# Kernel tuning notes

Hardware: AMD Instinct MI355X
Metric: run time of the kernel (lower is better)

## Reference

```python
import jax, jax.numpy as jnp
import numpy as np

B, N, D = 8, 2048, 1024
DC = 1024          # d_center
K = 4              # num_centers
NUM_JUMPS = 2
SPAN = 2
FIN = (2 + 2 * NUM_JUMPS + 1) * D  # 7*D

def _gelu(x):
    return jax.nn.gelu(x, approximate=False)  # torch nn.GELU default is exact erf

def setup_inputs() -> dict:
    key = jax.random.key(0)
    ks = jax.random.split(key, 16)
    s = lambda k, *sh: jax.random.normal(k, sh, dtype=jnp.float32) * 0.02
    return {
        "queries": jax.random.normal(ks[0], (B, N, D), dtype=jnp.float32),
        "fr_w1": s(ks[1], FIN, D), "fr_b1": jnp.zeros((D,), jnp.float32),
        "fr_w2": s(ks[2], D, D),   "fr_b2": jnp.zeros((D,), jnp.float32),
        "tc_w1": s(ks[3], D, DC),  "tc_b1": jnp.zeros((DC,), jnp.float32),
        "tc_w2": s(ks[4], DC, DC), "tc_b2": jnp.zeros((DC,), jnp.float32),
        "centers": jax.random.normal(ks[5], (K, DC), dtype=jnp.float32),
        "fc_w1": s(ks[6], D + DC, D), "fc_b1": jnp.zeros((D,), jnp.float32),
        "fc_w2": s(ks[7], D, D),      "fc_b2": jnp.zeros((D,), jnp.float32),
        "g_w": s(ks[8], D + DC, D),   "g_b": jnp.zeros((D,), jnp.float32),
    }

def reference(queries, fr_w1, fr_b1, fr_w2, fr_b2,
              tc_w1, tc_b1, tc_w2, tc_b2, centers,
              fc_w1, fc_b1, fc_w2, fc_b2, g_w, g_b):
    x = queries
    shifts = [1, -1, 0]  # left, right, x
    for i in range(1, NUM_JUMPS + 1):
        shifts += [i * SPAN, -i * SPAN]
    fusion = jnp.concatenate([jnp.roll(x, s, axis=1) for s in shifts], axis=-1)  # [B,N,7D]
    x_ring = _gelu(fusion @ fr_w1 + fr_b1) @ fr_w2 + fr_b2                       # [B,N,D]
    token_proj = _gelu(x_ring @ tc_w1 + tc_b1) @ tc_w2 + tc_b2                   # [B,N,DC]
    w = jax.nn.softmax(jnp.einsum('bnd,kd->bnk', token_proj, centers), axis=-1)  # [B,N,K]
    weighted = jnp.einsum('bnk,kd->bnd', w, centers)                             # [B,N,DC]
    fus2 = jnp.concatenate([x_ring, weighted], axis=-1)                          # [B,N,D+DC]
    gate = jax.nn.sigmoid(fus2 @ g_w + g_b)
    fc = _gelu(fus2 @ fc_w1 + fc_b1) @ fc_w2 + fc_b2
    return gate * fc + (1.0 - gate) * x_ring
```

## Files before the change

kernel.cpp:

```cpp
#include <hip/hip_runtime.h>
#include <hip/hip_bf16.h>
#include <math.h>

typedef unsigned short u16;
typedef __attribute__((ext_vector_type(8))) short short8;
typedef __attribute__((ext_vector_type(4))) float f32x4;


__device__ __forceinline__ float bf2f(u16 b) {
  return __uint_as_float(((unsigned int)b) << 16);
}
__device__ __forceinline__ u16 f2bf(float f) {
  unsigned int u = __float_as_uint(f);
  u += 0x7FFFu + ((u >> 16) & 1u);
  return (u16)(u >> 16);
}
__device__ __forceinline__ float gelu_exact(float x) {
  return 0.5f * x * (1.0f + erff(x * 0.70710678118654752f));
}

__device__ __forceinline__ void cp16(const void* g, void* l) {
  __builtin_amdgcn_global_load_lds(
      (const __attribute__((address_space(1))) unsigned int*)g,
      (__attribute__((address_space(3))) unsigned int*)l, 16, 0, 0);
}

template <int MODE, bool GATHER>
__global__ __launch_bounds__(256) void gemm128(
    const u16* __restrict__ A, int lda, const u16* __restrict__ Wt, int K,
    const float* __restrict__ bias, const float* __restrict__ bias2,
    void* __restrict__ out0, int ldo0, void* __restrict__ out1,
    void* __restrict__ out2, const float* __restrict__ p0,
    const float* __restrict__ p1, const float* __restrict__ p2) {
  __shared__ __align__(16) u16 As[128 * 64];
  __shared__ __align__(16) u16 Bs[128 * 64];

  const int tid = threadIdx.x;
  const int lane = tid & 63;
  const int wave = tid >> 6;
  const int wm = wave >> 1;
  const int wn = wave & 1;

  const unsigned linear = blockIdx.y * gridDim.x + blockIdx.x;
  const unsigned xcd = linear & 7u;
  const unsigned pos = linear >> 3;
  const unsigned bx = pos % gridDim.x;
  const unsigned by = xcd * (gridDim.y >> 3) + pos / gridDim.x;
  const int m0 = by * 128;
  const int n0 = bx * 128;

  const int srow = lane >> 3;
  const int sq = lane & 7;
  const int sqs = sq ^ srow;

  f32x4 acc[4][4];
#pragma unroll
  for (int i = 0; i < 4; i++)
#pragma unroll
    for (int j = 0; j < 4; j++) acc[i][j] = (f32x4){0.f, 0.f, 0.f, 0.f};

  for (int k0 = 0; k0 < K; k0 += 64) {
#pragma unroll
    for (int i = 0; i < 4; i++) {
      const int rloc = wave * 32 + i * 8 + srow;
      long gofs;
      if (GATHER) {
        const int seg = k0 >> 10;
        int shift;
        switch (seg) {
          case 0: shift = 1; break;
          case 1: shift = -1; break;
          case 2: shift = 0; break;
          case 3: shift = 2; break;
          case 4: shift = -2; break;
          case 5: shift = 4; break;
          default: shift = -4; break;
        }
        const int m = m0 + rloc;
        const int b = m >> 11;
        const int nsrc = ((m & 2047) - shift) & 2047;
        gofs = (long)((b << 11) | nsrc) * 1024 + (k0 & 1023) + sqs * 8;
      } else {
        gofs = (long)(m0 + rloc) * lda + k0 + sqs * 8;
      }
      cp16(A + gofs, &As[(wave * 32 + i * 8) * 64]);
    }
#pragma unroll
    for (int i = 0; i < 4; i++) {
      const int rloc = wave * 32 + i * 8 + srow;
      const long gofs = (long)(n0 + rloc) * K + k0 + sqs * 8;
      cp16(Wt + gofs, &Bs[(wave * 32 + i * 8) * 64]);
    }
    __syncthreads();

    const int q4 = lane >> 4;
    const int r16 = lane & 15;
#pragma unroll
    for (int kk = 0; kk < 2; kk++) {
      short8 af[4], bf[4];
#pragma unroll
      for (int mi = 0; mi < 4; mi++) {
        const int row = wm * 64 + mi * 16 + r16;
        const int q = (kk * 4 + q4) ^ (row & 7);
        af[mi] = *(const short8*)&As[row * 64 + q * 8];
      }
#pragma unroll
      for (int ni = 0; ni < 4; ni++) {
        const int row = wn * 64 + ni * 16 + r16;
        const int q = (kk * 4 + q4) ^ (row & 7);
        bf[ni] = *(const short8*)&Bs[row * 64 + q * 8];
      }
#pragma unroll
      for (int mi = 0; mi < 4; mi++)
#pragma unroll
        for (int ni = 0; ni < 4; ni++)
          acc[mi][ni] = __builtin_amdgcn_mfma_f32_16x16x32_bf16(
              af[mi], bf[ni], acc[mi][ni], 0, 0, 0);
    }
    __syncthreads();
  }

  const int ccol = lane & 15;
  const int crow = (lane >> 4) * 4;
#pragma unroll
  for (int mi = 0; mi < 4; mi++) {
#pragma unroll
    for (int r = 0; r < 4; r++) {
      const int m = m0 + wm * 64 + mi * 16 + crow + r;
      float4 wrow;
      if (MODE == 8) wrow = *(const float4*)(p0 + (size_t)m * 4);
#pragma unroll
      for (int ni = 0; ni < 4; ni++) {
        const int n = n0 + wn * 64 + ni * 16 + ccol;
        const float v = acc[mi][ni][r];
        if (MODE == 0) {
          ((u16*)out0)[(long)m * ldo0 + n] = f2bf(gelu_exact(v + bias[n]));
        } else if (MODE == 4) {
          const float g = p0[(long)m * 1024 + n];
          const float xr = p1[(long)m * 1024 + n];
          ((float*)out0)[(long)m * ldo0 + n] =
              g * (v + bias[n]) + (1.0f - g) * xr;
        } else if (MODE == 6) {
          ((u16*)out0)[(long)m * ldo0 + n] = f2bf(v);
        } else if (MODE == 7) {
          if (n < 1024) {
            const float s = v + bias[n];
            ((float*)out1)[(long)m * 1024 + n] = s;
            ((u16*)out0)[(long)m * 1024 + n] = f2bf(s);
          } else {
            const int nn = n - 1024;
            ((u16*)out2)[(long)m * 1024 + nn] = f2bf(gelu_exact(v + bias2[nn]));
          }
        } else if (MODE == 8) {
          if (n < 1024) {
            const float4 g2 = *(const float4*)(p1 + (size_t)n * 4);
            const float s = v + bias[n] + wrow.x * g2.x + wrow.y * g2.y +
                            wrow.z * g2.z + wrow.w * g2.w;
            ((float*)out0)[(long)m * 1024 + n] = 1.0f / (1.0f + expf(-s));
          } else {
            const int nn = n - 1024;
            const float4 f2 = *(const float4*)(p2 + (size_t)nn * 4);
            const float s = v + bias2[nn] + wrow.x * f2.x + wrow.y * f2.y +
                            wrow.z * f2.z + wrow.w * f2.w;
            ((u16*)out1)[(long)m * 1024 + nn] = f2bf(gelu_exact(s));
          }
        }
      }
    }
  }
}

__global__ __launch_bounds__(256) void cast_bf16(const float* __restrict__ in,
                                                 u16* __restrict__ out, int n4) {
  const long i = (long)blockIdx.x * 256 + threadIdx.x;
  if (i < n4) {
    const float4 v = ((const float4*)in)[i];
    ushort4 o;
    o.x = f2bf(v.x); o.y = f2bf(v.y); o.z = f2bf(v.z); o.w = f2bf(v.w);
    ((ushort4*)out)[i] = o;
  }
}

__global__ __launch_bounds__(256) void transp_bf16(const float* __restrict__ in,
                                                   u16* __restrict__ out, int K,
                                                   int N) {
  __shared__ float tile[32][33];
  const int tx = threadIdx.x & 31;
  const int ty = threadIdx.x >> 5;
  const long r0 = (long)blockIdx.y * 32;
  const long c0 = (long)blockIdx.x * 32;
#pragma unroll
  for (int r = 0; r < 4; r++)
    tile[ty + r * 8][tx] = in[(r0 + ty + r * 8) * N + c0 + tx];
  __syncthreads();
#pragma unroll
  for (int r = 0; r < 4; r++)
    out[(c0 + ty + r * 8) * K + r0 + tx] = f2bf(tile[tx][ty + r * 8]);
}

__global__ __launch_bounds__(256) void fold_all(
    const u16* __restrict__ GbT, const u16* __restrict__ FbT,
    const u16* __restrict__ Wt3, const float* __restrict__ centers,
    const float* __restrict__ fr_b2, const float* __restrict__ tc_b1,
    const float* __restrict__ tc_w2, const float* __restrict__ tc_b2,
    float* __restrict__ G2T, float* __restrict__ F2T, float* __restrict__ c2,
    float* __restrict__ S, float* __restrict__ bc) {
  const int b = blockIdx.x;
  const int wave = threadIdx.x >> 6, lane = threadIdx.x & 63;
  if (b < 256) {
    const int n = b * 4 + wave;
    float g[4] = {0.f, 0.f, 0.f, 0.f}, f[4] = {0.f, 0.f, 0.f, 0.f};
#pragma unroll
    for (int p = 0; p < 2; p++) {
      const int base = p * 512 + lane * 8;
      const short8 gv = *(const short8*)(GbT + (long)n * 1024 + base);
      const short8 fv = *(const short8*)(FbT + (long)n * 1024 + base);
#pragma unroll
      for (int e = 0; e < 8; e++) {
        const float ge = bf2f((u16)gv[e]), fe = bf2f((u16)fv[e]);
#pragma unroll
        for (int k = 0; k < 4; k++) {
          const float c = centers[k * 1024 + base + e];
          g[k] += ge * c;
          f[k] += fe * c;
        }
      }
    }
#pragma unroll
    for (int k = 0; k < 4; k++)
#pragma unroll
      for (int off = 32; off > 0; off >>= 1) {
        g[k] += __shfl_xor(g[k], off);
        f[k] += __shfl_xor(f[k], off);
      }
    if (lane == 0) {
#pragma unroll
      for (int k = 0; k < 4; k++) {
        G2T[n * 4 + k] = g[k];
        F2T[n * 4 + k] = f[k];
      }
    }
  } else if (b < 512) {
    const int j = (b - 256) * 4 + wave;
    float s = 0.f;
#pragma unroll
    for (int p = 0; p < 2; p++) {
      const int base = p * 512 + lane * 8;
      const short8 wv = *(const short8*)(Wt3 + (long)j * 1024 + base);
#pragma unroll
      for (int e = 0; e < 8; e++) s += fr_b2[base + e] * bf2f((u16)wv[e]);
    }
#pragma unroll
    for (int off = 32; off > 0; off >>= 1) s += __shfl_xor(s, off);
    if (lane == 0) c2[j] = s + tc_b1[j];
  } else if (b < 768) {
    const int d = (b - 512) * 4 + wave;
    const float* row = tc_w2 + (long)d * 1024;
    float s0 = 0.f, s1 = 0.f, s2 = 0.f, s3 = 0.f;
    for (int e = lane; e < 1024; e += 64) {
      const float w = row[e];
      s0 += w * centers[e];
      s1 += w * centers[1024 + e];
      s2 += w * centers[2048 + e];
      s3 += w * centers[3072 + e];
    }
#pragma unroll
    for (int off = 32; off > 0; off >>= 1) {
      s0 += __shfl_xor(s0, off);
      s1 += __shfl_xor(s1, off);
      s2 += __shfl_xor(s2, off);
      s3 += __shfl_xor(s3, off);
    }
    if (lane == 0) {
      S[d] = s0; S[1024 + d] = s1; S[2048 + d] = s2; S[3072 + d] = s3;
    }
  } else {
    const int k = wave;
    float s = 0.f;
    for (int e = lane; e < 1024; e += 64) s += tc_b2[e] * centers[k * 1024 + e];
#pragma unroll
    for (int off = 32; off > 0; off >>= 1) s += __shfl_xor(s, off);
    if (lane == 0) bc[k] = s;
  }
}

__global__ __launch_bounds__(256) void centers_kernel(
    const u16* __restrict__ h2, const float* __restrict__ S,
    const float* __restrict__ bc, float* __restrict__ wtok) {
  const int lane = threadIdx.x & 63;
  const int wave = threadIdx.x >> 6;
  const long t = (long)blockIdx.x * 4 + wave;
  const u16* row = h2 + t * 1024;
  float d0 = 0.f, d1 = 0.f, d2 = 0.f, d3 = 0.f;
#pragma unroll
  for (int j = 0; j < 2; j++) {
    const int dbase = j * 512 + lane * 8;
    const short8 v = *(const short8*)(row + dbase);
#pragma unroll
    for (int e = 0; e < 8; e++) {
      const float x = bf2f((u16)v[e]);
      const int d = dbase + e;
      d0 += x * S[d];
      d1 += x * S[1024 + d];
      d2 += x * S[2048 + d];
      d3 += x * S[3072 + d];
    }
  }
#pragma unroll
  for (int off = 32; off > 0; off >>= 1) {
    d0 += __shfl_xor(d0, off);
    d1 += __shfl_xor(d1, off);
    d2 += __shfl_xor(d2, off);
    d3 += __shfl_xor(d3, off);
  }
  if (lane == 0) {
    d0 += bc[0]; d1 += bc[1]; d2 += bc[2]; d3 += bc[3];
    const float mx = fmaxf(fmaxf(d0, d1), fmaxf(d2, d3));
    float e0 = expf(d0 - mx), e1 = expf(d1 - mx), e2 = expf(d2 - mx),
          e3 = expf(d3 - mx);
    const float inv = 1.0f / (e0 + e1 + e2 + e3);
    *(float4*)(wtok + t * 4) = (float4){e0 * inv, e1 * inv, e2 * inv, e3 * inv};
  }
}

extern "C" void kernel_launch(void* const* d_in, const int* in_sizes, int n_in,
                              void* d_out, int out_size, void* d_ws,
                              size_t ws_size, hipStream_t stream) {
  const float* queries = (const float*)d_in[0];
  const float* fr_w1 = (const float*)d_in[1];
  const float* fr_b1 = (const float*)d_in[2];
  const float* fr_w2 = (const float*)d_in[3];
  const float* fr_b2 = (const float*)d_in[4];
  const float* tc_w1 = (const float*)d_in[5];
  const float* tc_b1 = (const float*)d_in[6];
  const float* tc_w2 = (const float*)d_in[7];
  const float* tc_b2 = (const float*)d_in[8];
  const float* centers = (const float*)d_in[9];
  const float* fc_w1 = (const float*)d_in[10];
  const float* fc_b1 = (const float*)d_in[11];
  const float* fc_w2 = (const float*)d_in[12];
  const float* fc_b2 = (const float*)d_in[13];
  const float* g_w = (const float*)d_in[14];
  const float* g_b = (const float*)d_in[15];

  char* ws = (char*)d_ws;
  u16* Wt1 = (u16*)ws; ws += (size_t)7168 * 1024 * 2;
  u16* Wt3 = (u16*)ws; ws += (size_t)1024 * 1024 * 2;
  u16* Wt6 = (u16*)ws; ws += (size_t)1024 * 1024 * 2;
  u16* WtJ = (u16*)ws; ws += (size_t)2048 * 1024 * 2;
  u16* WtG2 = (u16*)ws; ws += (size_t)2048 * 1024 * 2;
  u16* Fw2b = (u16*)ws; ws += (size_t)1024 * 1024 * 2;
  u16* GbT = (u16*)ws; ws += (size_t)1024 * 1024 * 2;
  u16* FbT = (u16*)ws; ws += (size_t)1024 * 1024 * 2;
  u16* Xb = (u16*)ws;  ws += (size_t)16384 * 1024 * 2;
  u16* h1 = (u16*)ws;  ws += (size_t)16384 * 1024 * 2;
  u16* xrb = (u16*)ws; ws += (size_t)16384 * 1024 * 2;
  float* xring = (float*)ws; ws += (size_t)16384 * 1024 * 4;
  float* wtok = (float*)ws; ws += (size_t)16384 * 4 * 4;
  float* S = (float*)ws; ws += (size_t)4 * 1024 * 4;
  float* G2T = (float*)ws; ws += (size_t)1024 * 4 * 4;
  float* F2T = (float*)ws; ws += (size_t)1024 * 4 * 4;
  float* c2 = (float*)ws; ws += (size_t)1024 * 4;
  float* bc = (float*)ws; ws += 16;
  float* gate = (float*)d_out;
  float* out = (float*)d_out;

  cast_bf16<<<16384, 256, 0, stream>>>(queries, Xb, 16384 * 1024 / 4);
  cast_bf16<<<1024, 256, 0, stream>>>(fr_w2, Fw2b, 1024 * 1024 / 4);
  transp_bf16<<<dim3(32, 224), 256, 0, stream>>>(fr_w1, Wt1, 7168, 1024);
  transp_bf16<<<dim3(32, 32), 256, 0, stream>>>(tc_w1, Wt3, 1024, 1024);
  transp_bf16<<<dim3(32, 32), 256, 0, stream>>>(fc_w2, Wt6, 1024, 1024);
  transp_bf16<<<dim3(32, 32), 256, 0, stream>>>(fr_w2, WtJ, 1024, 1024);
  transp_bf16<<<dim3(32, 32), 256, 0, stream>>>(g_w, WtG2, 1024, 1024);
  transp_bf16<<<dim3(32, 32), 256, 0, stream>>>(fc_w1,
                                                WtG2 + (size_t)1024 * 1024,
                                                1024, 1024);
  transp_bf16<<<dim3(32, 32), 256, 0, stream>>>(g_w + (size_t)1024 * 1024, GbT,
                                                1024, 1024);
  transp_bf16<<<dim3(32, 32), 256, 0, stream>>>(fc_w1 + (size_t)1024 * 1024,
                                                FbT, 1024, 1024);
  fold_all<<<769, 256, 0, stream>>>(GbT, FbT, Wt3, centers, fr_b2, tc_b1,
                                    tc_w2, tc_b2, G2T, F2T, c2, S, bc);
  gemm128<6, false><<<dim3(8, 8), 256, 0, stream>>>(
      Wt3, 1024, Fw2b, 1024, nullptr, nullptr, WtJ + (size_t)1024 * 1024, 1024,
      nullptr, nullptr, nullptr, nullptr, nullptr);

  gemm128<0, true><<<dim3(8, 128), 256, 0, stream>>>(
      Xb, 0, Wt1, 7168, fr_b1, nullptr, h1, 1024, nullptr, nullptr, nullptr,
      nullptr, nullptr);
  gemm128<7, false><<<dim3(16, 128), 256, 0, stream>>>(
      h1, 1024, WtJ, 1024, fr_b2, c2, xrb, 1024, xring, Xb, nullptr, nullptr,
      nullptr);
  centers_kernel<<<4096, 256, 0, stream>>>(Xb, S, bc, wtok);
  gemm128<8, false><<<dim3(16, 128), 256, 0, stream>>>(
      xrb, 1024, WtG2, 1024, g_b, fc_b1, gate, 1024, h1, nullptr, wtok, G2T,
      F2T);
  gemm128<4, false><<<dim3(8, 128), 256, 0, stream>>>(
      h1, 1024, Wt6, 1024, fc_b2, nullptr, out, 1024, nullptr, nullptr, gate,
      xring, nullptr);
}
```

Measured before the change: 880.7 us.

## Double-buffer GEMM LDS tiles and merge weight-prep launches into one kernel

```diff
diff --git a/kernel.cpp b/kernel.cpp
--- a/kernel.cpp
+++ b/kernel.cpp
@@ -32,8 +32,10 @@
     void* __restrict__ out0, int ldo0, void* __restrict__ out1,
     void* __restrict__ out2, const float* __restrict__ p0,
     const float* __restrict__ p1, const float* __restrict__ p2) {
-  __shared__ __align__(16) u16 As[128 * 64];
-  __shared__ __align__(16) u16 Bs[128 * 64];
+  __shared__ __align__(16) u16 As0[128 * 64];
+  __shared__ __align__(16) u16 Bs0[128 * 64];
+  __shared__ __align__(16) u16 As1[128 * 64];
+  __shared__ __align__(16) u16 Bs1[128 * 64];
 
   const int tid = threadIdx.x;
   const int lane = tid & 63;
@@ -59,7 +61,7 @@
 #pragma unroll
     for (int j = 0; j < 4; j++) acc[i][j] = (f32x4){0.f, 0.f, 0.f, 0.f};
 
-  for (int k0 = 0; k0 < K; k0 += 64) {
+  auto stageA = [&](int k0, u16* buf) {
 #pragma unroll
     for (int i = 0; i < 4; i++) {
       const int rloc = wave * 32 + i * 8 + srow;
@@ -83,18 +85,32 @@
       } else {
         gofs = (long)(m0 + rloc) * lda + k0 + sqs * 8;
       }
-      cp16(A + gofs, &As[(wave * 32 + i * 8) * 64]);
-    }
+      cp16(A + gofs, &buf[(wave * 32 + i * 8) * 64]);
+    }
+  };
+  auto stageB = [&](int k0, u16* buf) {
 #pragma unroll
     for (int i = 0; i < 4; i++) {
       const int rloc = wave * 32 + i * 8 + srow;
       const long gofs = (long)(n0 + rloc) * K + k0 + sqs * 8;
-      cp16(Wt + gofs, &Bs[(wave * 32 + i * 8) * 64]);
-    }
-    __syncthreads();
-
-    const int q4 = lane >> 4;
-    const int r16 = lane & 15;
+      cp16(Wt + gofs, &buf[(wave * 32 + i * 8) * 64]);
+    }
+  };
+
+  const int niter = K >> 6;
+  stageA(0, As0);
+  stageB(0, Bs0);
+  u16* ar = As0; u16* br = Bs0;
+  u16* aw = As1; u16* bw = Bs1;
+  __syncthreads();
+
+  const int q4 = lane >> 4;
+  const int r16 = lane & 15;
+  for (int it = 0; it < niter; ++it) {
+    if (it + 1 < niter) {
+      stageA((it + 1) << 6, aw);
+      stageB((it + 1) << 6, bw);
+    }
 #pragma unroll
     for (int kk = 0; kk < 2; kk++) {
       short8 af[4], bf[4];
@@ -102,13 +118,13 @@
       for (int mi = 0; mi < 4; mi++) {
         const int row = wm * 64 + mi * 16 + r16;
         const int q = (kk * 4 + q4) ^ (row & 7);
-        af[mi] = *(const short8*)&As[row * 64 + q * 8];
+        af[mi] = *(const short8*)&ar[row * 64 + q * 8];
       }
 #pragma unroll
       for (int ni = 0; ni < 4; ni++) {
         const int row = wn * 64 + ni * 16 + r16;
         const int q = (kk * 4 + q4) ^ (row & 7);
-        bf[ni] = *(const short8*)&Bs[row * 64 + q * 8];
+        bf[ni] = *(const short8*)&br[row * 64 + q * 8];
       }
 #pragma unroll
       for (int mi = 0; mi < 4; mi++)
@@ -118,10 +134,13 @@
               af[mi], bf[ni], acc[mi][ni], 0, 0, 0);
     }
     __syncthreads();
-  }
-
-  const int ccol = lane & 15;
-  const int crow = (lane >> 4) * 4;
+    u16* t;
+    t = ar; ar = aw; aw = t;
+    t = br; br = bw; bw = t;
+  }
+
+  const int ccol = r16;
+  const int crow = q4 * 4;
 #pragma unroll
   for (int mi = 0; mi < 4; mi++) {
 #pragma unroll
@@ -181,14 +200,14 @@
   }
 }
 
-__global__ __launch_bounds__(256) void transp_bf16(const float* __restrict__ in,
-                                                   u16* __restrict__ out, int K,
-                                                   int N) {
-  __shared__ float tile[32][33];
-  const int tx = threadIdx.x & 31;
-  const int ty = threadIdx.x >> 5;
-  const long r0 = (long)blockIdx.y * 32;
-  const long c0 = (long)blockIdx.x * 32;
+__device__ __forceinline__ void transp_tile(const float* __restrict__ in,
+                                            u16* __restrict__ out, int K, int N,
+                                            int bx, int by, float (*tile)[33],
+                                            int tid) {
+  const int tx = tid & 31;
+  const int ty = tid >> 5;
+  const long r0 = (long)by * 32;
+  const long c0 = (long)bx * 32;
 #pragma unroll
   for (int r = 0; r < 4; r++)
     tile[ty + r * 8][tx] = in[(r0 + ty + r * 8) * N + c0 + tx];
@@ -198,63 +217,77 @@
     out[(c0 + ty + r * 8) * K + r0 + tx] = f2bf(tile[tx][ty + r * 8]);
 }
 
+__global__ __launch_bounds__(256) void prep_all(
+    const float* __restrict__ fr_w1, const float* __restrict__ fr_w2,
+    const float* __restrict__ tc_w1, const float* __restrict__ fc_w2,
+    const float* __restrict__ g_w, const float* __restrict__ fc_w1,
+    u16* __restrict__ Wt1, u16* __restrict__ WtJ, u16* __restrict__ Wt3,
+    u16* __restrict__ Wt6, u16* __restrict__ WtG2, u16* __restrict__ Fw2b) {
+  __shared__ float tile[32][33];
+  const int b = blockIdx.x;
+  const int tid = threadIdx.x;
+  if (b < 7168) {
+    transp_tile(fr_w1, Wt1, 7168, 1024, b & 31, b >> 5, tile, tid);
+  } else if (b < 8192) {
+    const int t = b - 7168;
+    transp_tile(fr_w2, WtJ, 1024, 1024, t & 31, t >> 5, tile, tid);
+  } else if (b < 9216) {
+    const int t = b - 8192;
+    transp_tile(tc_w1, Wt3, 1024, 1024, t & 31, t >> 5, tile, tid);
+  } else if (b < 10240) {
+    const int t = b - 9216;
+    transp_tile(fc_w2, Wt6, 1024, 1024, t & 31, t >> 5, tile, tid);
+  } else if (b < 11264) {
+    const int t = b - 10240;
+    transp_tile(g_w, WtG2, 1024, 1024, t & 31, t >> 5, tile, tid);
+  } else if (b < 12288) {
+    const int t = b - 11264;
+    transp_tile(fc_w1, WtG2 + (size_t)1024 * 1024, 1024, 1024, t & 31, t >> 5,
+                tile, tid);
+  } else {
+    const long i = (long)(b - 12288) * 256 + tid;
+    const float4 v = ((const float4*)fr_w2)[i];
+    ushort4 o;
+    o.x = f2bf(v.x); o.y = f2bf(v.y); o.z = f2bf(v.z); o.w = f2bf(v.w);
+    ((ushort4*)Fw2b)[i] = o;
+  }
+}
+
 __global__ __launch_bounds__(256) void fold_all(
-    const u16* __restrict__ GbT, const u16* __restrict__ FbT,
-    const u16* __restrict__ Wt3, const float* __restrict__ centers,
+    const float* __restrict__ g_w, const float* __restrict__ fc_w1,
+    const float* __restrict__ tc_w1, const float* __restrict__ centers,
     const float* __restrict__ fr_b2, const float* __restrict__ tc_b1,
     const float* __restrict__ tc_w2, const float* __restrict__ tc_b2,
     float* __restrict__ G2T, float* __restrict__ F2T, float* __restrict__ c2,
     float* __restrict__ S, float* __restrict__ bc) {
   const int b = blockIdx.x;
-  const int wave = threadIdx.x >> 6, lane = threadIdx.x & 63;
-  if (b < 256) {
-    const int n = b * 4 + wave;
+  const int tid = threadIdx.x;
+  if (b < 4) {
+    const int n = b * 256 + tid;
     float g[4] = {0.f, 0.f, 0.f, 0.f}, f[4] = {0.f, 0.f, 0.f, 0.f};
-#pragma unroll
-    for (int p = 0; p < 2; p++) {
-      const int base = p * 512 + lane * 8;
-      const short8 gv = *(const short8*)(GbT + (long)n * 1024 + base);
-      const short8 fv = *(const short8*)(FbT + (long)n * 1024 + base);
-#pragma unroll
-      for (int e = 0; e < 8; e++) {
-        const float ge = bf2f((u16)gv[e]), fe = bf2f((u16)fv[e]);
-#pragma unroll
-        for (int k = 0; k < 4; k++) {
-          const float c = centers[k * 1024 + base + e];
-          g[k] += ge * c;
-          f[k] += fe * c;
-        }
+    for (int e = 0; e < 1024; e++) {
+      const float gv = g_w[(size_t)(1024 + e) * 1024 + n];
+      const float fv = fc_w1[(size_t)(1024 + e) * 1024 + n];
+#pragma unroll
+      for (int k = 0; k < 4; k++) {
+        const float c = centers[k * 1024 + e];
+        g[k] += gv * c;
+        f[k] += fv * c;
       }
     }
 #pragma unroll
-    for (int k = 0; k < 4; k++)
-#pragma unroll
-      for (int off = 32; off > 0; off >>= 1) {
-        g[k] += __shfl_xor(g[k], off);
-        f[k] += __shfl_xor(f[k], off);
-      }
-    if (lane == 0) {
-#pragma unroll
-      for (int k = 0; k < 4; k++) {
-        G2T[n * 4 + k] = g[k];
-        F2T[n * 4 + k] = f[k];
-      }
-    }
-  } else if (b < 512) {
-    const int j = (b - 256) * 4 + wave;
+    for (int k = 0; k < 4; k++) {
+      G2T[n * 4 + k] = g[k];
+      F2T[n * 4 + k] = f[k];
+    }
+  } else if (b < 8) {
+    const int j = (b - 4) * 256 + tid;
     float s = 0.f;
-#pragma unroll
-    for (int p = 0; p < 2; p++) {
-      const int base = p * 512 + lane * 8;
-      const short8 wv = *(const short8*)(Wt3 + (long)j * 1024 + base);
-#pragma unroll
-      for (int e = 0; e < 8; e++) s += fr_b2[base + e] * bf2f((u16)wv[e]);
-    }
-#pragma unroll
-    for (int off = 32; off > 0; off >>= 1) s += __shfl_xor(s, off);
-    if (lane == 0) c2[j] = s + tc_b1[j];
-  } else if (b < 768) {
-    const int d = (b - 512) * 4 + wave;
+    for (int e = 0; e < 1024; e++) s += fr_b2[e] * tc_w1[(size_t)e * 1024 + j];
+    c2[j] = s + tc_b1[j];
+  } else if (b < 264) {
+    const int wave = tid >> 6, lane = tid & 63;
+    const int d = (b - 8) * 4 + wave;
     const float* row = tc_w2 + (long)d * 1024;
     float s0 = 0.f, s1 = 0.f, s2 = 0.f, s3 = 0.f;
     for (int e = lane; e < 1024; e += 64) {
@@ -275,6 +308,7 @@
       S[d] = s0; S[1024 + d] = s1; S[2048 + d] = s2; S[3072 + d] = s3;
     }
   } else {
+    const int wave = tid >> 6, lane = tid & 63;
     const int k = wave;
     float s = 0.f;
     for (int e = lane; e < 1024; e += 64) s += tc_b2[e] * centers[k * 1024 + e];
@@ -350,8 +384,6 @@
   u16* WtJ = (u16*)ws; ws += (size_t)2048 * 1024 * 2;
   u16* WtG2 = (u16*)ws; ws += (size_t)2048 * 1024 * 2;
   u16* Fw2b = (u16*)ws; ws += (size_t)1024 * 1024 * 2;
-  u16* GbT = (u16*)ws; ws += (size_t)1024 * 1024 * 2;
-  u16* FbT = (u16*)ws; ws += (size_t)1024 * 1024 * 2;
   u16* Xb = (u16*)ws;  ws += (size_t)16384 * 1024 * 2;
   u16* h1 = (u16*)ws;  ws += (size_t)16384 * 1024 * 2;
   u16* xrb = (u16*)ws; ws += (size_t)16384 * 1024 * 2;
@@ -366,20 +398,9 @@
   float* out = (float*)d_out;
 
   cast_bf16<<<16384, 256, 0, stream>>>(queries, Xb, 16384 * 1024 / 4);
-  cast_bf16<<<1024, 256, 0, stream>>>(fr_w2, Fw2b, 1024 * 1024 / 4);
-  transp_bf16<<<dim3(32, 224), 256, 0, stream>>>(fr_w1, Wt1, 7168, 1024);
-  transp_bf16<<<dim3(32, 32), 256, 0, stream>>>(tc_w1, Wt3, 1024, 1024);
-  transp_bf16<<<dim3(32, 32), 256, 0, stream>>>(fc_w2, Wt6, 1024, 1024);
-  transp_bf16<<<dim3(32, 32), 256, 0, stream>>>(fr_w2, WtJ, 1024, 1024);
-  transp_bf16<<<dim3(32, 32), 256, 0, stream>>>(g_w, WtG2, 1024, 1024);
-  transp_bf16<<<dim3(32, 32), 256, 0, stream>>>(fc_w1,
-                                                WtG2 + (size_t)1024 * 1024,
-                                                1024, 1024);
-  transp_bf16<<<dim3(32, 32), 256, 0, stream>>>(g_w + (size_t)1024 * 1024, GbT,
-                                                1024, 1024);
-  transp_bf16<<<dim3(32, 32), 256, 0, stream>>>(fc_w1 + (size_t)1024 * 1024,
-                                                FbT, 1024, 1024);
-  fold_all<<<769, 256, 0, stream>>>(GbT, FbT, Wt3, centers, fr_b2, tc_b1,
+  prep_all<<<13312, 256, 0, stream>>>(fr_w1, fr_w2, tc_w1, fc_w2, g_w, fc_w1,
+                                      Wt1, WtJ, Wt3, Wt6, WtG2, Fw2b);
+  fold_all<<<265, 256, 0, stream>>>(g_w, fc_w1, tc_w1, centers, fr_b2, tc_b1,
                                     tc_w2, tc_b2, G2T, F2T, c2, S, bc);
   gemm128<6, false><<<dim3(8, 8), 256, 0, stream>>>(
       Wt3, 1024, Fw2b, 1024, nullptr, nullptr, WtJ + (size_t)1024 * 1024, 1024,
```

Measured after the change: 1.021 ms. 1.16x slower.
